# Kernel optimization log

Measured on AMD Instinct MI355X. Metric: run time of the kernel, lower is better.

Reference implementation:

```python
import jax, jax.numpy as jnp
import numpy as np

B, T, N, H, E = 4, 64, 4096, 128, 65536


def setup_inputs() -> dict:
    key = jax.random.key(0)
    ks = jax.random.split(key, 16)
    s = 1.0 / np.sqrt(H)
    u = lambda k, shape: jax.random.uniform(k, shape, jnp.float32, -s, s)
    return {
        "x": jax.random.normal(ks[0], (B, T, N, H), jnp.float32),
        "targets": jax.random.normal(ks[1], (B, T, N, 1), jnp.float32),
        "W_msg": u(ks[2], (H, H)),
        "b_msg": u(ks[3], (H,)),
        "W_mix": u(ks[4], (2 * H, H)),
        "b_mix": u(ks[5], (H,)),
        "W_ih": u(ks[6], (H, 3 * H)),
        "b_ih": u(ks[7], (3 * H,)),
        "W_hh": u(ks[8], (H, 3 * H)),
        "b_hh": u(ks[9], (3 * H,)),
        "W_ro": u(ks[10], (H, 1)),
        "b_ro": u(ks[11], (1,)),
        "targets_mask": jax.random.randint(ks[12], (B, T, N, 1), 0, 2) > 0,
        "edge_src": jax.random.randint(ks[13], (E,), 0, N),
        "edge_dst": jax.random.randint(ks[14], (E,), 0, N),
    }


def reference(x, targets, W_msg, b_msg, W_mix, b_mix, W_ih, b_ih, W_hh, b_hh,
              W_ro, b_ro, targets_mask, edge_src, edge_dst):
    def step(state, x_t):  # state: [B,N,H] (carried 'inputs'), x_t: [B,N,H]
        # GraphRNN: message from node state (here x_t), scatter-add over edges
        m = x_t @ W_msg + b_msg                                   # [B,N,H]
        agg = jnp.zeros_like(m).at[:, edge_dst].add(m[:, edge_src])  # sum aggr
        # mix aggregated messages with 'inputs' (the carried state)
        mi = jnp.concatenate([agg, state], axis=-1) @ W_mix + b_mix  # [B,N,H]
        # GRUCell(input=mi, hidden=x_t)
        gi = mi @ W_ih + b_ih                                     # [B,N,3H]
        gh = x_t @ W_hh + b_hh
        i_r, i_z, i_n = jnp.split(gi, 3, axis=-1)
        h_r, h_z, h_n = jnp.split(gh, 3, axis=-1)
        r = jax.nn.sigmoid(i_r + h_r)
        z = jax.nn.sigmoid(i_z + h_z)
        n = jnp.tanh(i_n + r * h_n)
        new_state = (1.0 - z) * n + z * x_t                       # [B,N,H]
        out = new_state @ W_ro + b_ro                             # [B,N,1]
        return new_state, out

    state0 = jnp.zeros((x.shape[0], x.shape[2], x.shape[3]), x.dtype)
    _, outs = jax.lax.scan(step, state0, jnp.swapaxes(x, 0, 1))   # [T,B,N,1]
    outputs = jnp.moveaxis(outs, 0, 1)                            # [B,T,N,1]
    mse = 0.5 * (outputs - targets) ** 2
    mask = targets_mask.astype(mse.dtype)
    return jnp.sum(mse * mask) / jnp.sum(mask)
```

## Files before the change

### kernel.cpp

```cpp
#include <hip/hip_runtime.h>
#include <hip/hip_bf16.h>
#include <stdint.h>

#define BB 4
#define TT 64
#define NN 4096
#define HH 128
#define EE 65536
#define BN (BB*NN)

typedef __attribute__((ext_vector_type(8))) short short8;
typedef __attribute__((ext_vector_type(4))) float f32x4;

__device__ __forceinline__ unsigned short bf16r(float f) {
    unsigned u = __float_as_uint(f);
    u += 0x7fffu + ((u >> 16) & 1u);
    return (unsigned short)(u >> 16);
}
__device__ __forceinline__ unsigned cvt_pk_bf16(float lo_, float hi_) {
    unsigned r;
    asm("v_cvt_pk_bf16_f32 %0, %1, %2" : "=v"(r) : "v"(lo_), "v"(hi_));
    return r;
}
__device__ __forceinline__ unsigned short bf16s(float f) {
    unsigned r;
    asm("v_cvt_pk_bf16_f32 %0, %1, %1" : "=v"(r) : "v"(f));
    return (unsigned short)r;
}
__device__ __forceinline__ float bf2f(unsigned bits16) {
    return __uint_as_float(bits16 << 16);
}
__device__ __forceinline__ float sigm(float x) { return 1.f / (1.f + __expf(-x)); }
__device__ __forceinline__ float tanhfast(float x) {
    return 1.f - 2.f / (__expf(2.f * x) + 1.f);
}
__device__ __forceinline__ unsigned swz(int row, int colbyte) {
    return (unsigned)(row * 256 + (colbyte ^ ((row & 7) << 4)));
}

#define GLD_LDS16(g, s) __builtin_amdgcn_global_load_lds( \
    (const __attribute__((address_space(1))) void*)(g), \
    (__attribute__((address_space(3))) void*)(s), 16, 0, 0)

__global__ void pack_wc_kernel(const float* __restrict__ W_msg, const float* __restrict__ W_mix,
                               float* __restrict__ Wc)
{
    int idx = blockIdx.x * 256 + threadIdx.x;
    int k = idx >> 7, j = idx & 127;
    float s = 0.f;
    for (int i = 0; i < 128; ++i) s += W_msg[k * 128 + i] * W_mix[i * 128 + j];
    Wc[idx] = s;
}

__global__ void pack_bvec_kernel(const float* __restrict__ b_msg, const float* __restrict__ W_mix,
                                 float* __restrict__ bvec)
{
    int j = threadIdx.x;
    float s = 0.f;
    for (int i = 0; i < 128; ++i) s += b_msg[i] * W_mix[i * 128 + j];
    bvec[j] = s;
}

__global__ void pack_gbias_kernel(const float* __restrict__ bvec, const float* __restrict__ b_mix,
                                  const float* __restrict__ W_ih, const float* __restrict__ b_ih,
                                  const float* __restrict__ b_hh,
                                  float* __restrict__ gvec, float* __restrict__ cvec)
{
    int c = threadIdx.x;
    float g = 0.f, gb = 0.f;
    for (int j = 0; j < 128; ++j) {
        g  += bvec[j]  * W_ih[j * 384 + c];
        gb += b_mix[j] * W_ih[j * 384 + c];
    }
    gvec[c] = g;
    cvec[c] = gb + b_ih[c] + (c < 256 ? b_hh[c] : 0.f);
}

__global__ void pack_G_kernel(const float* __restrict__ Wc, const float* __restrict__ W_mix,
                              const float* __restrict__ W_ih, const float* __restrict__ W_hh,
                              short* __restrict__ Gp)
{
    int idx = blockIdx.x * 256 + threadIdx.x;
    if (idx >= 18432) return;
    int l = idx & 63, ks = (idx >> 6) & 3, nt = (idx >> 8) & 7, mat = idx >> 11;
    int lo = l & 15, hi = l >> 4;
    int col = nt * 16 + lo;
    short8 v;
    #pragma unroll
    for (int i = 0; i < 8; ++i) {
        int k = ks * 32 + hi * 8 + i;
        float s;
        if (mat < 3) {
            int c = mat * 128 + col;
            s = 0.f;
            for (int j = 0; j < 128; ++j) s += Wc[k * 128 + j] * W_ih[j * 384 + c];
        } else if (mat < 6) {
            int c = (mat - 3) * 128 + col;
            s = 0.f;
            for (int j = 0; j < 128; ++j) s += W_mix[(128 + k) * 128 + j] * W_ih[j * 384 + c];
        } else {
            int c = (mat - 6) * 128 + col;
            s = W_hh[k * 384 + c];
        }
        v[i] = (short)bf16r(s);
    }
    *(short8*)(Gp + (size_t)idx * 8) = v;
}

__global__ void pack_wro_kernel(const float* __restrict__ W_ro, short* __restrict__ out)
{
    int idx = threadIdx.x;
    int l = idx & 63, ks = idx >> 6;
    int lo = l & 15, hi = l >> 4;
    short8 v;
    #pragma unroll
    for (int i = 0; i < 8; ++i) {
        int k = ks * 32 + hi * 8 + i;
        v[i] = (lo == 0) ? (short)bf16r(W_ro[k]) : (short)0;
    }
    *(short8*)(out + (size_t)idx * 8) = v;
}

__global__ __launch_bounds__(256)
void cvt_img_kernel(const float* __restrict__ x, char* __restrict__ img)
{
    int tileid = blockIdx.x;
    int phys = tileid >> 6, t = tileid & 63;
    int b = phys >> 6, n0 = (phys & 63) * 64;
    const float* __restrict__ src = x + ((size_t)(b * TT + t) * NN + n0) * HH;
    char* __restrict__ dst = img + (size_t)tileid * 32768;
    int tid = threadIdx.x;
    #pragma unroll
    for (int u4 = 0; u4 < 4; ++u4) {
        int unit = tid + u4 * 256;
        int row = unit >> 4, g = unit & 15;
        const float* sp = src + row * HH + g * 8;
        float4 v0 = *(const float4*)sp;
        float4 v1 = *(const float4*)(sp + 4);
        uint4 o;
        o.x = cvt_pk_bf16(v0.x, v0.y);
        o.y = cvt_pk_bf16(v0.z, v0.w);
        o.z = cvt_pk_bf16(v1.x, v1.y);
        o.w = cvt_pk_bf16(v1.z, v1.w);
        *(uint4*)(dst + swz(row, g * 16)) = o;
    }
}

__global__ __launch_bounds__(256)
void gather_quad_kernel(char* __restrict__ img,
                        const int* __restrict__ off, const int* __restrict__ srcs)
{
    int bid = blockIdx.x;
    int xcd = bid & 7;
    int rest = bid >> 3;
    int grp = rest >> 8;
    int chunk = rest & 255;
    int w = threadIdx.x >> 6, l = threadIdx.x & 63;
    int half = l >> 5, L = l & 31;
    size_t baseA, baseB;
    {
        int btA = (grp * 4 + half * 2 + 0) * 8 + xcd;
        int btB = (grp * 4 + half * 2 + 1) * 8 + xcd;
        baseA = ((size_t)(btA >> 6) * 4096 + (btA & 63)) * 32768;
        baseB = ((size_t)(btB >> 6) * 4096 + (btB & 63)) * 32768;
    }

    #pragma unroll
    for (int r = 0; r < 4; ++r) {
        int dst = chunk * 16 + w * 4 + r;
        int s = off[dst], e = off[dst + 1];
        float aA0 = 0.f, aA1 = 0.f, aA2 = 0.f, aA3 = 0.f;
        float aB0 = 0.f, aB1 = 0.f, aB2 = 0.f, aB3 = 0.f;
        int i = s;
        for (; i + 1 < e; i += 2) {
            int s0 = srcs[i], s1 = srcs[i + 1];
            size_t t0 = ((size_t)(s0 >> 6) << 21) + ((unsigned)(s0 & 63) << 8)
                      + ((L * 8) ^ ((s0 & 7) << 4));
            size_t t1 = ((size_t)(s1 >> 6) << 21) + ((unsigned)(s1 & 63) << 8)
                      + ((L * 8) ^ ((s1 & 7) << 4));
            uint2 vA0 = *(const uint2*)(img + baseA + t0);
            uint2 vB0 = *(const uint2*)(img + baseB + t0);
            uint2 vA1 = *(const uint2*)(img + baseA + t1);
            uint2 vB1 = *(const uint2*)(img + baseB + t1);
            aA0 += __uint_as_float(vA0.x << 16) + __uint_as_float(vA1.x << 16);
            aA1 += __uint_as_float(vA0.x & 0xffff0000u) + __uint_as_float(vA1.x & 0xffff0000u);
            aA2 += __uint_as_float(vA0.y << 16) + __uint_as_float(vA1.y << 16);
            aA3 += __uint_as_float(vA0.y & 0xffff0000u) + __uint_as_float(vA1.y & 0xffff0000u);
            aB0 += __uint_as_float(vB0.x << 16) + __uint_as_float(vB1.x << 16);
            aB1 += __uint_as_float(vB0.x & 0xffff0000u) + __uint_as_float(vB1.x & 0xffff0000u);
            aB2 += __uint_as_float(vB0.y << 16) + __uint_as_float(vB1.y << 16);
            aB3 += __uint_as_float(vB0.y & 0xffff0000u) + __uint_as_float(vB1.y & 0xffff0000u);
        }
        if (i < e) {
            int s0 = srcs[i];
            size_t t0 = ((size_t)(s0 >> 6) << 21) + ((unsigned)(s0 & 63) << 8)
                      + ((L * 8) ^ ((s0 & 7) << 4));
            uint2 vA0 = *(const uint2*)(img + baseA + t0);
            uint2 vB0 = *(const uint2*)(img + baseB + t0);
            aA0 += __uint_as_float(vA0.x << 16);
            aA1 += __uint_as_float(vA0.x & 0xffff0000u);
            aA2 += __uint_as_float(vA0.y << 16);
            aA3 += __uint_as_float(vA0.y & 0xffff0000u);
            aB0 += __uint_as_float(vB0.x << 16);
            aB1 += __uint_as_float(vB0.x & 0xffff0000u);
            aB2 += __uint_as_float(vB0.y << 16);
            aB3 += __uint_as_float(vB0.y & 0xffff0000u);
        }
        size_t doff = 16384 + ((size_t)(dst >> 6) << 21) + ((unsigned)(dst & 63) << 8)
                    + ((L * 8) ^ ((dst & 7) << 4));
        uint2 oA, oB;
        oA.x = cvt_pk_bf16(aA0, aA1);
        oA.y = cvt_pk_bf16(aA2, aA3);
        oB.x = cvt_pk_bf16(aB0, aB1);
        oB.y = cvt_pk_bf16(aB2, aB3);
        *(uint2*)(img + baseA + doff) = oA;
        *(uint2*)(img + baseB + doff) = oB;
    }
}

#define STEP10(T, SXC, SXN, SAC, SAN, SSC, SSN) { \
    const int t = (T); \
    float tgtNext = 0.f, mvNext = 0.f; \
    if (tid < 64) { \
        size_t ti = (size_t)(b * TT + t) * NN + n0 + tid; \
        tgtNext = targets[ti]; \
        mvNext = fl ? (((const unsigned char*)maskp)[ti] ? 1.f : 0.f) \
                    : (((const int*)maskp)[ti] ? 1.f : 0.f); \
    } \
     \
    if (t + 1 < TT) { \
        const char* g = img + tbase + (size_t)(t + 1) * 32768 + (w * 2) * 1024 + l * 16; \
        GLD_LDS16(g,                 (char*)SXN + (w * 2) * 1024); \
        GLD_LDS16(g + 1024,          (char*)SXN + (w * 2 + 1) * 1024); \
        GLD_LDS16(g + 16384,         (char*)SAN + (w * 2) * 1024); \
        GLD_LDS16(g + 16384 + 1024,  (char*)SAN + (w * 2 + 1) * 1024); \
    } \
    f32x4 R[4] = {}, Z[4] = {}, N4[4] = {}, H4[4] = {}; \
    _Pragma("unroll") \
    for (int ks = 0; ks < 4; ++ks) { \
        short8 af[4]; \
        _Pragma("unroll") \
        for (int s4 = 0; s4 < 4; ++s4) \
            af[s4] = *(const short8*)((const char*)SAC + swz(s4 * 16 + lo, ks * 64 + hi * 16)); \
        _Pragma("unroll") \
        for (int s4 = 0; s4 < 4; ++s4) \
            R[s4] = __builtin_amdgcn_mfma_f32_16x16x32_bf16(af[s4], wf[0][ks], R[s4], 0, 0, 0); \
        _Pragma("unroll") \
        for (int s4 = 0; s4 < 4; ++s4) \
            Z[s4] = __builtin_amdgcn_mfma_f32_16x16x32_bf16(af[s4], wf[1][ks], Z[s4], 0, 0, 0); \
        _Pragma("unroll") \
        for (int s4 = 0; s4 < 4; ++s4) \
            N4[s4] = __builtin_amdgcn_mfma_f32_16x16x32_bf16(af[s4], wf[2][ks], N4[s4], 0, 0, 0); \
    } \
    _Pragma("unroll") \
    for (int ks = 0; ks < 4; ++ks) { \
        short8 af[4]; \
        _Pragma("unroll") \
        for (int s4 = 0; s4 < 4; ++s4) \
            af[s4] = *(const short8*)((const char*)SSC + swz(s4 * 16 + lo, ks * 64 + hi * 16)); \
        _Pragma("unroll") \
        for (int s4 = 0; s4 < 4; ++s4) \
            R[s4] = __builtin_amdgcn_mfma_f32_16x16x32_bf16(af[s4], wf[3][ks], R[s4], 0, 0, 0); \
        _Pragma("unroll") \
        for (int s4 = 0; s4 < 4; ++s4) \
            Z[s4] = __builtin_amdgcn_mfma_f32_16x16x32_bf16(af[s4], wf[4][ks], Z[s4], 0, 0, 0); \
        _Pragma("unroll") \
        for (int s4 = 0; s4 < 4; ++s4) \
            N4[s4] = __builtin_amdgcn_mfma_f32_16x16x32_bf16(af[s4], wf[5][ks], N4[s4], 0, 0, 0); \
    } \
    _Pragma("unroll") \
    for (int ks = 0; ks < 4; ++ks) { \
        short8 af[4]; \
        _Pragma("unroll") \
        for (int s4 = 0; s4 < 4; ++s4) \
            af[s4] = *(const short8*)((const char*)SXC + swz(s4 * 16 + lo, ks * 64 + hi * 16)); \
        _Pragma("unroll") \
        for (int s4 = 0; s4 < 4; ++s4) \
            R[s4] = __builtin_amdgcn_mfma_f32_16x16x32_bf16(af[s4], wf[6][ks], R[s4], 0, 0, 0); \
        _Pragma("unroll") \
        for (int s4 = 0; s4 < 4; ++s4) \
            Z[s4] = __builtin_amdgcn_mfma_f32_16x16x32_bf16(af[s4], wf[7][ks], Z[s4], 0, 0, 0); \
        _Pragma("unroll") \
        for (int s4 = 0; s4 < 4; ++s4) \
            H4[s4] = __builtin_amdgcn_mfma_f32_16x16x32_bf16(af[s4], wf[8][ks], H4[s4], 0, 0, 0); \
    } \
    _Pragma("unroll") \
    for (int s4 = 0; s4 < 4; ++s4) \
        _Pragma("unroll") \
        for (int q = 0; q < 4; ++q) { \
            int row = s4 * 16 + hi * 4 + q; \
            float dg = sdeg[row]; \
            float rv = sigm(R[s4][q] + fmaf(dg, gvR, cR)); \
            float zv = sigm(Z[s4][q] + fmaf(dg, gvZ, cZ)); \
            float nv = tanhfast(N4[s4][q] + fmaf(dg, gvN, cN) + rv * (H4[s4][q] + bH)); \
            float xv = bf2f(*(const unsigned short*)((const char*)SXC + swz(row, jcol * 2))); \
            float ns = fmaf(zv, xv - nv, nv); \
            *(unsigned short*)((char*)SSN + swz(row, jcol * 2)) = bf16s(ns); \
        } \
    __syncthreads();    \
    if (w < 4) { \
        f32x4 acc = {}; \
        _Pragma("unroll") \
        for (int ks = 0; ks < 4; ++ks) { \
            short8 af = *(const short8*)((const char*)SSN + swz(w * 16 + lo, ks * 64 + hi * 16)); \
            short8 bw = *(const short8*)(WroP + (size_t)(ks * 64 + l) * 8); \
            acc = __builtin_amdgcn_mfma_f32_16x16x32_bf16(af, bw, acc, 0, 0, 0); \
        } \
        if (lo == 0) { \
            _Pragma("unroll") \
            for (int q = 0; q < 4; ++q) \
                pOut[t & 1][w * 16 + hi * 4 + q] = acc[q]; \
        } \
    } \
    if (tid < 64 && t > 0) { \
        float out = pOut[(t & 1) ^ 1][tid] + bro; \
        float d = out - tgtCur; \
        lossAcc += 0.5f * d * d * mvCur; \
    } \
    tgtCur = tgtNext; mvCur = mvNext; \
}

__global__ __launch_bounds__(512, 2)
void mega10_kernel(const char* __restrict__ img,
                   const short* __restrict__ Gp, const short* __restrict__ WroP,
                   const float* __restrict__ degf,
                   const float* __restrict__ gvec, const float* __restrict__ cvec,
                   const float* __restrict__ b_hh, const float* __restrict__ b_ro,
                   const float* __restrict__ targets, const void* __restrict__ maskp,
                   const int* __restrict__ flag,
                   float* __restrict__ lossBlock)
{
    __shared__ char sX0[16384];
    __shared__ char sX1[16384];
    __shared__ char sA0[16384];
    __shared__ char sA1[16384];
    __shared__ char sS0[16384];
    __shared__ char sS1[16384];
    __shared__ float sdeg[64];
    __shared__ float pOut[2][64];
    __shared__ float pLoss[8];

    const int tid = threadIdx.x;
    const int w = tid >> 6, l = tid & 63, lo = l & 15, hi = l >> 4;
    const int nt = w;
    const int phys = blockIdx.x;
    const int b = phys >> 6;
    const int n0 = (phys & 63) * 64;
    const size_t tbase = (size_t)phys * TT * 32768;

    short8 wf[9][4];
    #pragma unroll
    for (int m = 0; m < 9; ++m)
        #pragma unroll
        for (int ks = 0; ks < 4; ++ks)
            wf[m][ks] = *(const short8*)(Gp + (size_t)(((m * 8 + nt) * 4 + ks) * 64 + l) * 8);

    const int jcol = nt * 16 + lo;
    const float gvR = gvec[jcol], gvZ = gvec[128 + jcol], gvN = gvec[256 + jcol];
    const float cR = cvec[jcol], cZ = cvec[128 + jcol], cN = cvec[256 + jcol];
    const float bH = b_hh[256 + jcol];
    const float bro = b_ro[0];
    const int fl = *flag;

    {
        const char* g = img + tbase + (w * 2) * 1024 + l * 16;
        GLD_LDS16(g,                sX0 + (w * 2) * 1024);
        GLD_LDS16(g + 1024,         sX0 + (w * 2 + 1) * 1024);
        GLD_LDS16(g + 16384,        sA0 + (w * 2) * 1024);
        GLD_LDS16(g + 16384 + 1024, sA0 + (w * 2 + 1) * 1024);
    }
    #pragma unroll
    for (int it = 0; it < 8; ++it) ((unsigned*)sS0)[tid + it * 512] = 0u;
    if (tid < 64) sdeg[tid] = degf[n0 + tid];
    float tgtCur = 0.f, mvCur = 0.f, lossAcc = 0.f;
    __syncthreads();

    for (int tt = 0; tt < TT; tt += 2) {
        STEP10(tt,     sX0, sX1, sA0, sA1, sS0, sS1)
        STEP10(tt + 1, sX1, sX0, sA1, sA0, sS1, sS0)
    }

    __syncthreads();
    if (tid < 64) {
        float out = pOut[1][tid] + bro;
        float d = out - tgtCur;
        lossAcc += 0.5f * d * d * mvCur;
    }

    float v = lossAcc;
    #pragma unroll
    for (int o = 1; o < 64; o <<= 1) v += __shfl_xor(v, o);
    if (l == 0) pLoss[w] = v;
    __syncthreads();
    if (tid == 0) {
        float s = 0.f;
        #pragma unroll
        for (int ww = 0; ww < 8; ++ww) s += pLoss[ww];
        lossBlock[phys] = s;
    }
}

__global__ void count_kernel(const int* __restrict__ dst, int* __restrict__ counts)
{
    int e = blockIdx.x * 256 + threadIdx.x;
    if (e < EE) atomicAdd(&counts[dst[e]], 1);
}

__global__ __launch_bounds__(1024)
void scan_kernel(const int* __restrict__ counts, int* __restrict__ off, int* __restrict__ cursor,
                 float* __restrict__ degf)
{
    __shared__ int s[1024];
    int tid = threadIdx.x;
    int base = tid * 4;
    int c[4]; int sum = 0;
    #pragma unroll
    for (int i = 0; i < 4; ++i) { c[i] = counts[base + i]; sum += c[i]; }
    s[tid] = sum; __syncthreads();
    for (int o = 1; o < 1024; o <<= 1) {
        int v = (tid >= o) ? s[tid - o] : 0;
        __syncthreads();
        s[tid] += v;
        __syncthreads();
    }
    int incl = s[tid];
    int run = incl - sum;
    #pragma unroll
    for (int i = 0; i < 4; ++i) {
        off[base + i] = run; cursor[base + i] = run;
        degf[base + i] = (float)c[i];
        run += c[i];
    }
    if (tid == 1023) off[4096] = incl;
}

__global__ void fill_kernel(const int* __restrict__ src, const int* __restrict__ dst,
                            int* __restrict__ cursor, int* __restrict__ csr_src)
{
    int e = blockIdx.x * 256 + threadIdx.x;
    if (e < EE) {
        int d = dst[e];
        int pos = atomicAdd(&cursor[d], 1);
        csr_src[pos] = src[e];
    }
}

__global__ void detect_kernel(const unsigned char* __restrict__ maskb, int* __restrict__ flag)
{
    int i = blockIdx.x * 256 + threadIdx.x;
    bool hit = (i < BB * TT * NN) && (i & 3) && maskb[i];
    if (__any(hit) && (threadIdx.x & 63) == 0) atomicOr(flag, 1);
}

__global__ void masksum_kernel(const void* __restrict__ maskp, const int* __restrict__ flag,
                               float* __restrict__ den)
{
    int i = blockIdx.x * 256 + threadIdx.x;
    float v = 0.f;
    if (i < BB * TT * NN) {
        if (*flag) v = ((const unsigned char*)maskp)[i] ? 1.f : 0.f;
        else       v = ((const int*)maskp)[i] ? 1.f : 0.f;
    }
    #pragma unroll
    for (int o = 32; o > 0; o >>= 1) v += __shfl_down(v, o);
    __shared__ float sm[4];
    if ((threadIdx.x & 63) == 0) sm[threadIdx.x >> 6] = v;
    __syncthreads();
    if (threadIdx.x == 0) atomicAdd(den, sm[0] + sm[1] + sm[2] + sm[3]);
}

__global__ __launch_bounds__(256)
void final_kernel(const float* __restrict__ lossBlock, const float* __restrict__ den,
                  unsigned* __restrict__ out)
{
    __shared__ float s[256];
    s[threadIdx.x] = lossBlock[threadIdx.x];
    __syncthreads();
    for (int o = 128; o > 0; o >>= 1) {
        if (threadIdx.x < o) s[threadIdx.x] += s[threadIdx.x + o];
        __syncthreads();
    }
    if (threadIdx.x == 0) {
        float L = s[0] / den[0];
        unsigned u = __float_as_uint(L);
        u += 0x7fffu + ((u >> 16) & 1u);
        unsigned hi = u >> 16;
        out[0] = hi * 0x10001u;
    }
}

extern "C" void kernel_launch(void* const* d_in, const int* in_sizes, int n_in,
                              void* d_out, int out_size, void* d_ws, size_t ws_size,
                              hipStream_t stream)
{
    const float* x       = (const float*)d_in[0];
    const float* targets = (const float*)d_in[1];
    const float* W_msg   = (const float*)d_in[2];
    const float* b_msg   = (const float*)d_in[3];
    const float* W_mix   = (const float*)d_in[4];
    const float* b_mix   = (const float*)d_in[5];
    const float* W_ih    = (const float*)d_in[6];
    const float* b_ih    = (const float*)d_in[7];
    const float* W_hh    = (const float*)d_in[8];
    const float* b_hh    = (const float*)d_in[9];
    const float* W_ro    = (const float*)d_in[10];
    const float* b_ro    = (const float*)d_in[11];
    const void*  maskp   = d_in[12];
    const int*   esrc    = (const int*)d_in[13];
    const int*   edst    = (const int*)d_in[14];

    char* ws = (char*)d_ws;
    char* img = ws; ws += (size_t)256 * TT * 32768;
    short* Gp          = (short*)ws; ws += (size_t)18432 * 8 * 2;
    short* WroP        = (short*)ws; ws += (size_t)256 * 8 * 2;
    float* Wc_f32      = (float*)ws; ws += 16384 * 4;
    float* bvec        = (float*)ws; ws += 128 * 4;
    float* gvec        = (float*)ws; ws += 384 * 4;
    float* cvec        = (float*)ws; ws += 384 * 4;
    float* degf        = (float*)ws; ws += 4096 * 4;
    float* lossBlock   = (float*)ws; ws += 256 * 4;
    int*   csr_off     = (int*)ws;   ws += 4104 * 4;
    int*   cursor      = (int*)ws;   ws += 4096 * 4;
    int*   counts      = (int*)ws;   ws += 4096 * 4;
    int*   csr_src     = (int*)ws;   ws += (size_t)EE * 4;
    int*   flag        = (int*)ws;   ws += 64;
    float* den         = (float*)ws; ws += 64;

    hipMemsetAsync(counts, 0, 4096 * 4, stream);
    hipMemsetAsync(flag, 0, 64, stream);
    hipMemsetAsync(den, 0, 4, stream);

    detect_kernel   <<<4096, 256, 0, stream>>>((const unsigned char*)maskp, flag);
    masksum_kernel  <<<4096, 256, 0, stream>>>(maskp, flag, den);
    count_kernel    <<<EE / 256, 256, 0, stream>>>(edst, counts);
    scan_kernel     <<<1, 1024, 0, stream>>>(counts, csr_off, cursor, degf);
    fill_kernel     <<<EE / 256, 256, 0, stream>>>(esrc, edst, cursor, csr_src);
    pack_wc_kernel  <<<64, 256, 0, stream>>>(W_msg, W_mix, Wc_f32);
    pack_bvec_kernel<<<1, 128, 0, stream>>>(b_msg, W_mix, bvec);
    pack_gbias_kernel<<<1, 384, 0, stream>>>(bvec, b_mix, W_ih, b_ih, b_hh, gvec, cvec);
    pack_G_kernel   <<<72, 256, 0, stream>>>(Wc_f32, W_mix, W_ih, W_hh, Gp);
    pack_wro_kernel <<<1, 256, 0, stream>>>(W_ro, WroP);

    cvt_img_kernel  <<<16384, 256, 0, stream>>>(x, img);
    gather_quad_kernel<<<16384, 256, 0, stream>>>(img, csr_off, csr_src);

    mega10_kernel<<<256, 512, 0, stream>>>(img, Gp, WroP, degf, gvec, cvec, b_hh, b_ro,
                                           targets, maskp, flag, lossBlock);
    final_kernel<<<1, 256, 0, stream>>>(lossBlock, den, (unsigned*)d_out);
}
```

Measured before the change: 1.262 ms.

## Widen LDS swizzle, unroll edge gather by four, split readout across all waves

Widens the XOR swizzle from 8 to 16 rows in both the shared-memory layout and the global image addressing, so that LDS reads of 16-row MFMA fragments should hit fewer bank conflicts. Unrolls the CSR gather loop to four edges per iteration to keep more independent loads in flight. The readout MFMA is split across all 8 waves by K-half, with the two partial sums added when the loss is computed. Any producer of the image outside the visible code must use the same swizzle, otherwise results will be wrong.

```diff
diff --git a/kernel.cpp b/kernel.cpp
--- a/kernel.cpp
+++ b/kernel.cpp
@@ -35,7 +35,7 @@
     return 1.f - 2.f / (__expf(2.f * x) + 1.f);
 }
 __device__ __forceinline__ unsigned swz(int row, int colbyte) {
-    return (unsigned)(row * 256 + (colbyte ^ ((row & 7) << 4)));
+    return (unsigned)(row * 256 + (colbyte ^ ((row & 15) << 4)));
 }
 
 #define GLD_LDS16(g, s) __builtin_amdgcn_global_load_lds( \
@@ -172,29 +172,45 @@
         float aA0 = 0.f, aA1 = 0.f, aA2 = 0.f, aA3 = 0.f;
         float aB0 = 0.f, aB1 = 0.f, aB2 = 0.f, aB3 = 0.f;
         int i = s;
-        for (; i + 1 < e; i += 2) {
-            int s0 = srcs[i], s1 = srcs[i + 1];
+        for (; i + 3 < e; i += 4) {
+            int s0 = srcs[i], s1 = srcs[i + 1], s2 = srcs[i + 2], s3 = srcs[i + 3];
             size_t t0 = ((size_t)(s0 >> 6) << 21) + ((unsigned)(s0 & 63) << 8)
-                      + ((L * 8) ^ ((s0 & 7) << 4));
+                      + ((L * 8) ^ ((s0 & 15) << 4));
             size_t t1 = ((size_t)(s1 >> 6) << 21) + ((unsigned)(s1 & 63) << 8)
-                      + ((L * 8) ^ ((s1 & 7) << 4));
+                      + ((L * 8) ^ ((s1 & 15) << 4));
+            size_t t2 = ((size_t)(s2 >> 6) << 21) + ((unsigned)(s2 & 63) << 8)
+                      + ((L * 8) ^ ((s2 & 15) << 4));
+            size_t t3 = ((size_t)(s3 >> 6) << 21) + ((unsigned)(s3 & 63) << 8)
+                      + ((L * 8) ^ ((s3 & 15) << 4));
             uint2 vA0 = *(const uint2*)(img + baseA + t0);
             uint2 vB0 = *(const uint2*)(img + baseB + t0);
             uint2 vA1 = *(const uint2*)(img + baseA + t1);
             uint2 vB1 = *(const uint2*)(img + baseB + t1);
-            aA0 += __uint_as_float(vA0.x << 16) + __uint_as_float(vA1.x << 16);
-            aA1 += __uint_as_float(vA0.x & 0xffff0000u) + __uint_as_float(vA1.x & 0xffff0000u);
-            aA2 += __uint_as_float(vA0.y << 16) + __uint_as_float(vA1.y << 16);
-            aA3 += __uint_as_float(vA0.y & 0xffff0000u) + __uint_as_float(vA1.y & 0xffff0000u);
-            aB0 += __uint_as_float(vB0.x << 16) + __uint_as_float(vB1.x << 16);
-            aB1 += __uint_as_float(vB0.x & 0xffff0000u) + __uint_as_float(vB1.x & 0xffff0000u);
-            aB2 += __uint_as_float(vB0.y << 16) + __uint_as_float(vB1.y << 16);
-            aB3 += __uint_as_float(vB0.y & 0xffff0000u) + __uint_as_float(vB1.y & 0xffff0000u);
+            uint2 vA2 = *(const uint2*)(img + baseA + t2);
+            uint2 vB2 = *(const uint2*)(img + baseB + t2);
+            uint2 vA3 = *(const uint2*)(img + baseA + t3);
+            uint2 vB3 = *(const uint2*)(img + baseB + t3);
+            aA0 += (__uint_as_float(vA0.x << 16) + __uint_as_float(vA1.x << 16))
+                 + (__uint_as_float(vA2.x << 16) + __uint_as_float(vA3.x << 16));
+            aA1 += (__uint_as_float(vA0.x & 0xffff0000u) + __uint_as_float(vA1.x & 0xffff0000u))
+                 + (__uint_as_float(vA2.x & 0xffff0000u) + __uint_as_float(vA3.x & 0xffff0000u));
+            aA2 += (__uint_as_float(vA0.y << 16) + __uint_as_float(vA1.y << 16))
+                 + (__uint_as_float(vA2.y << 16) + __uint_as_float(vA3.y << 16));
+            aA3 += (__uint_as_float(vA0.y & 0xffff0000u) + __uint_as_float(vA1.y & 0xffff0000u))
+                 + (__uint_as_float(vA2.y & 0xffff0000u) + __uint_as_float(vA3.y & 0xffff0000u));
+            aB0 += (__uint_as_float(vB0.x << 16) + __uint_as_float(vB1.x << 16))
+                 + (__uint_as_float(vB2.x << 16) + __uint_as_float(vB3.x << 16));
+            aB1 += (__uint_as_float(vB0.x & 0xffff0000u) + __uint_as_float(vB1.x & 0xffff0000u))
+                 + (__uint_as_float(vB2.x & 0xffff0000u) + __uint_as_float(vB3.x & 0xffff0000u));
+            aB2 += (__uint_as_float(vB0.y << 16) + __uint_as_float(vB1.y << 16))
+                 + (__uint_as_float(vB2.y << 16) + __uint_as_float(vB3.y << 16));
+            aB3 += (__uint_as_float(vB0.y & 0xffff0000u) + __uint_as_float(vB1.y & 0xffff0000u))
+                 + (__uint_as_float(vB2.y & 0xffff0000u) + __uint_as_float(vB3.y & 0xffff0000u));
         }
-        if (i < e) {
+        for (; i < e; ++i) {
             int s0 = srcs[i];
             size_t t0 = ((size_t)(s0 >> 6) << 21) + ((unsigned)(s0 & 63) << 8)
-                      + ((L * 8) ^ ((s0 & 7) << 4));
+                      + ((L * 8) ^ ((s0 & 15) << 4));
             uint2 vA0 = *(const uint2*)(img + baseA + t0);
             uint2 vB0 = *(const uint2*)(img + baseB + t0);
             aA0 += __uint_as_float(vA0.x << 16);
@@ -207,7 +223,7 @@
             aB3 += __uint_as_float(vB0.y & 0xffff0000u);
         }
         size_t doff = 16384 + ((size_t)(dst >> 6) << 21) + ((unsigned)(dst & 63) << 8)
-                    + ((L * 8) ^ ((dst & 7) << 4));
+                    + ((L * 8) ^ ((dst & 15) << 4));
         uint2 oA, oB;
         oA.x = cvt_pk_bf16(aA0, aA1);
         oA.y = cvt_pk_bf16(aA2, aA3);
@@ -227,7 +243,6 @@
         mvNext = fl ? (((const unsigned char*)maskp)[ti] ? 1.f : 0.f) \
                     : (((const int*)maskp)[ti] ? 1.f : 0.f); \
     } \
-     \
     if (t + 1 < TT) { \
         const char* g = img + tbase + (size_t)(t + 1) * 32768 + (w * 2) * 1024 + l * 16; \
         GLD_LDS16(g,                 (char*)SXN + (w * 2) * 1024); \
@@ -298,22 +313,24 @@
             *(unsigned short*)((char*)SSN + swz(row, jcol * 2)) = bf16s(ns); \
         } \
     __syncthreads();    \
-    if (w < 4) { \
+    { \
+        const int band = w & 3, khalf = w >> 2; \
         f32x4 acc = {}; \
         _Pragma("unroll") \
-        for (int ks = 0; ks < 4; ++ks) { \
-            short8 af = *(const short8*)((const char*)SSN + swz(w * 16 + lo, ks * 64 + hi * 16)); \
+        for (int kk = 0; kk < 2; ++kk) { \
+            int ks = khalf * 2 + kk; \
+            short8 af = *(const short8*)((const char*)SSN + swz(band * 16 + lo, ks * 64 + hi * 16)); \
             short8 bw = *(const short8*)(WroP + (size_t)(ks * 64 + l) * 8); \
             acc = __builtin_amdgcn_mfma_f32_16x16x32_bf16(af, bw, acc, 0, 0, 0); \
         } \
         if (lo == 0) { \
             _Pragma("unroll") \
             for (int q = 0; q < 4; ++q) \
-                pOut[t & 1][w * 16 + hi * 4 + q] = acc[q]; \
+                pOut[t & 1][khalf][band * 16 + hi * 4 + q] = acc[q]; \
         } \
     } \
     if (tid < 64 && t > 0) { \
-        float out = pOut[(t & 1) ^ 1][tid] + bro; \
+        float out = pOut[(t & 1) ^ 1][0][tid] + pOut[(t & 1) ^ 1][1][tid] + bro; \
         float d = out - tgtCur; \
         lossAcc += 0.5f * d * d * mvCur; \
     } \
@@ -337,7 +354,7 @@
     __shared__ char sS0[16384];
     __shared__ char sS1[16384];
     __shared__ float sdeg[64];
-    __shared__ float pOut[2][64];
+    __shared__ float pOut[2][2][64];
     __shared__ float pLoss[8];
 
     const int tid = threadIdx.x;
@@ -382,7 +399,7 @@
 
     __syncthreads();
     if (tid < 64) {
-        float out = pOut[1][tid] + bro;
+        float out = pOut[1][0][tid] + pOut[1][1][tid] + bro;
         float d = out - tgtCur;
         lossAcc += 0.5f * d * d * mvCur;
     }
```

Result: faster. 1.214 ms (-3.8%).
